# Kernel optimization log

Hardware: AMD Instinct MI355X
Metric: run time of the kernel (lower is better)

Reference implementation:

```python
import jax, jax.numpy as jnp
import numpy as np


def setup_inputs() -> dict:
    key = jax.random.key(0)
    k1, k2 = jax.random.split(key)
    B, N, M = 16, 4096, 4096
    x1 = jax.random.normal(k1, (B, N, 3), dtype=jnp.float32)
    x2 = jax.random.normal(k2, (B, M, 3), dtype=jnp.float32)
    return {"x1": x1, "x2": x2}


def reference(x1, x2) -> jnp.ndarray:
    # x1: [B, N, 3], x2: [B, M, 3]
    # dist_matrix[b, i, j] = ||x1[b,i] - x2[b,j]||^2 via |a|^2 + |b|^2 - 2 a.b
    x1_norm = jnp.sum(x1 * x1, axis=2, keepdims=True)           # [B, N, 1]
    x2_norm = jnp.sum(x2 * x2, axis=2)[:, None, :]              # [B, 1, M]
    cross = jnp.einsum('bnd,bmd->bnm', x1, x2)                  # [B, N, M]
    dist_matrix = x1_norm + x2_norm - 2.0 * cross               # [B, N, M]
    min_1_to_2 = jnp.min(dist_matrix, axis=2)                   # [B, N]
    min_2_to_1 = jnp.min(dist_matrix, axis=1)                   # [B, M]
    chamfer = jnp.mean(min_1_to_2, axis=1) + jnp.mean(min_2_to_1, axis=1)  # [B]
    return chamfer
```

## Files before the change

kernel.cpp:

```cpp
#include <hip/hip_runtime.h>


typedef __attribute__((ext_vector_type(8))) __bf16 bf16x8;
typedef __attribute__((ext_vector_type(16))) float f32x16;

#define PTS 4096
#define NB 16

__device__ __forceinline__ unsigned f2bf(float f) {
  unsigned u = __float_as_uint(f);
  return (u + 0x7FFFu + ((u >> 16) & 1u)) >> 16;
}
__device__ __forceinline__ float bf2f(unsigned s) {
  return __uint_as_float(s << 16);
}
__device__ __forceinline__ unsigned pk(unsigned lo, unsigned hi) {
  return (lo & 0xFFFFu) | (hi << 16);
}

__global__ __launch_bounds__(512, 2) void chamfer_main(
    const float* __restrict__ x1, const float* __restrict__ x2,
    float* __restrict__ rowpart) {
  const int s  = blockIdx.x;
  const int d  = s & 1;
  const int b  = (s >> 1) & (NB - 1);
  const int ch = (s >> 5) & 1;
  const int rg = blockIdx.y;

  const int tid  = threadIdx.x;
  const int lane = tid & 63;
  const int half = lane >> 5;
  const int l31  = lane & 31;
  const int wave = tid >> 6;

  __shared__ uint4 lds[4096];

  const float* Q = d ? x1 : x2;
  const int cbase = b * PTS + ch * 2048;
#pragma unroll
  for (int k = 0; k < 4; ++k) {
    const int j = tid + k * 512;
    const float* q = Q + (size_t)(cbase + j) * 3;
    const float x = q[0], y = q[1], z = q[2];
    const float sx = -2.f * x, sy = -2.f * y, sz = -2.f * z;
    const unsigned Hx = f2bf(sx), Hy = f2bf(sy), Hz = f2bf(sz);
    const unsigned Lx = f2bf(sx - bf2f(Hx));
    const unsigned Ly = f2bf(sy - bf2f(Hy));
    const unsigned Lz = f2bf(sz - bf2f(Hz));
    const float n = fmaf(x, x, fmaf(y, y, z * z));
    const unsigned nh = f2bf(n), nl = f2bf(n - bf2f(nh));
    const unsigned one = 0x3F80u;
    uint4 w0, w1;
    w0.x = pk(Hx, Hy); w0.y = pk(Hz, Lx); w0.z = pk(Ly, Lz); w0.w = pk(Hx, Hy);
    w1.x = pk(Hz, nh); w1.y = pk(nl, one); w1.z = pk(one, 0u); w1.w = 0u;
    lds[(j >> 5) * 64 + (j & 31)]      = w0;
    lds[(j >> 5) * 64 + 32 + (j & 31)] = w1;
  }

  const float* P = d ? x2 : x1;
  const int t0 = rg * 16 + wave * 2;
  bf16x8 af[2];
#pragma unroll
  for (int rr = 0; rr < 2; ++rr) {
    const int r = (t0 + rr) * 32 + l31;
    const float* p = P + (size_t)(b * PTS + r) * 3;
    const float x = p[0], y = p[1], zc = p[2];
    const unsigned hx = f2bf(x), hy = f2bf(y), hz = f2bf(zc);
    const unsigned lx = f2bf(x - bf2f(hx));
    const unsigned ly = f2bf(y - bf2f(hy));
    const unsigned lz = f2bf(zc - bf2f(hz));
    const float n = fmaf(x, x, fmaf(y, y, zc * zc));
    const unsigned nh = f2bf(n), nl = f2bf(n - bf2f(nh));
    const unsigned one = 0x3F80u;
    uint4 w0, w1;
    w0.x = pk(hx, hy); w0.y = pk(hz, hx); w0.z = pk(hy, hz); w0.w = pk(lx, ly);
    w1.x = pk(lz, one); w1.y = pk(one, nh); w1.z = pk(nl, 0u); w1.w = 0u;
    uint4 w;
    w.x = half ? w1.x : w0.x; w.y = half ? w1.y : w0.y;
    w.z = half ? w1.z : w0.z; w.w = half ? w1.w : w0.w;
    af[rr] = *(const bf16x8*)&w;
  }
  const bf16x8 af0 = af[0], af1 = af[1];

  f32x16 zero;
#pragma unroll
  for (int e = 0; e < 16; ++e) zero[e] = 0.f;

  float rm0[16], rm1[16];
#pragma unroll
  for (int e = 0; e < 16; ++e) { rm0[e] = 3.0e38f; rm1[e] = 3.0e38f; }

  __syncthreads();

  const uint4* tp = &lds[half * 32 + l31];
  bf16x8 buf[4];
  buf[0] = *(const bf16x8*)&tp[0];
  buf[1] = *(const bf16x8*)&tp[64];

#pragma unroll 2
  for (int g = 0; g < 32; ++g) {
    const int cur = (g & 1) * 2;
    const int nxt = ((g + 1) & 1) * 2;
    const int pf  = ((g + 1) & 31) * 2;
    buf[nxt]     = *(const bf16x8*)&tp[pf * 64];
    buf[nxt + 1] = *(const bf16x8*)&tp[(pf + 1) * 64];
    const bf16x8 b0 = buf[cur], b1 = buf[cur + 1];
    const f32x16 a00 =
        __builtin_amdgcn_mfma_f32_32x32x16_bf16(af0, b0, zero, 0, 0, 0);
    const f32x16 a01 =
        __builtin_amdgcn_mfma_f32_32x32x16_bf16(af0, b1, zero, 0, 0, 0);
#pragma unroll
    for (int e = 0; e < 16; ++e)
      rm0[e] = fminf(fminf(a00[e], a01[e]), rm0[e]);
    const f32x16 a10 =
        __builtin_amdgcn_mfma_f32_32x32x16_bf16(af1, b0, zero, 0, 0, 0);
    const f32x16 a11 =
        __builtin_amdgcn_mfma_f32_32x32x16_bf16(af1, b1, zero, 0, 0, 0);
#pragma unroll
    for (int e = 0; e < 16; ++e)
      rm1[e] = fminf(fminf(a10[e], a11[e]), rm1[e]);
  }

  float* rbase = rowpart + ((size_t)((ch * 2 + d) * NB + b)) * PTS + t0 * 32;
#pragma unroll
  for (int e = 0; e < 16; ++e) {
    float v = rm0[e];
    v = fminf(v, __shfl_xor(v, 1));
    v = fminf(v, __shfl_xor(v, 2));
    v = fminf(v, __shfl_xor(v, 4));
    v = fminf(v, __shfl_xor(v, 8));
    v = fminf(v, __shfl_xor(v, 16));
    if (l31 == e) {
      const int rl = (e & 3) + 8 * (e >> 2) + 4 * half;
      rbase[rl] = fmaxf(v, 0.f);
    }
  }
#pragma unroll
  for (int e = 0; e < 16; ++e) {
    float v = rm1[e];
    v = fminf(v, __shfl_xor(v, 1));
    v = fminf(v, __shfl_xor(v, 2));
    v = fminf(v, __shfl_xor(v, 4));
    v = fminf(v, __shfl_xor(v, 8));
    v = fminf(v, __shfl_xor(v, 16));
    if (l31 == e) {
      const int rl = 32 + (e & 3) + 8 * (e >> 2) + 4 * half;
      rbase[rl] = fmaxf(v, 0.f);
    }
  }
}

__global__ __launch_bounds__(512) void reduce_rows(
    const float* __restrict__ rowpart, float* __restrict__ out) {
  const int b = blockIdx.x;
  const int tid = threadIdx.x;
  const float* p0 = rowpart + (size_t)(0 * NB + b) * PTS;
  const float* p1 = rowpart + (size_t)(1 * NB + b) * PTS;
  const float* p2 = rowpart + (size_t)(2 * NB + b) * PTS;
  const float* p3 = rowpart + (size_t)(3 * NB + b) * PTS;
  float s = 0.f;
  for (int i = tid; i < PTS; i += 512)
    s += fminf(p0[i], p2[i]) + fminf(p1[i], p3[i]);
  s += __shfl_xor(s, 1);
  s += __shfl_xor(s, 2);
  s += __shfl_xor(s, 4);
  s += __shfl_xor(s, 8);
  s += __shfl_xor(s, 16);
  s += __shfl_xor(s, 32);
  __shared__ float acc[8];
  if ((tid & 63) == 0) acc[tid >> 6] = s;
  __syncthreads();
  if (tid == 0) {
    float t = 0.f;
#pragma unroll
    for (int w = 0; w < 8; ++w) t += acc[w];
    out[b] = t * (1.f / PTS);
  }
}

extern "C" void kernel_launch(void* const* d_in, const int* in_sizes, int n_in,
                              void* d_out, int out_size, void* d_ws,
                              size_t ws_size, hipStream_t stream) {
  const float* x1 = (const float*)d_in[0];
  const float* x2 = (const float*)d_in[1];
  float* out = (float*)d_out;

  float* rowpart = (float*)d_ws;

  dim3 grid(64, 8);
  chamfer_main<<<grid, 512, 0, stream>>>(x1, x2, rowpart);
  reduce_rows<<<NB, 512, 0, stream>>>(rowpart, out);
}
```

Measured before the change: 81.22 us.

## Fuse row reduction into main kernel via global atomic counter tail blocks

Removes the separate reduce_rows launch. Each block bumps a global counter after writing its row minima, and the last 16 arrivals wait for all 512 blocks to finish before reducing one batch each. This saves a kernel launch and its gap, at the cost of atomic stores and loads, a spin-wait, and the assumption that all blocks can make progress. The counter is never reset; it relies on wrapping in multiples of 512.

```diff
diff --git a/kernel.cpp b/kernel.cpp
--- a/kernel.cpp
+++ b/kernel.cpp
@@ -6,6 +6,8 @@
 
 #define PTS 4096
 #define NB 16
+
+__device__ unsigned g_cnt = 0;
 
 __device__ __forceinline__ unsigned f2bf(float f) {
   unsigned u = __float_as_uint(f);
@@ -18,9 +20,9 @@
   return (lo & 0xFFFFu) | (hi << 16);
 }
 
-__global__ __launch_bounds__(512, 2) void chamfer_main(
+__global__ __launch_bounds__(512, 2) void chamfer_all(
     const float* __restrict__ x1, const float* __restrict__ x2,
-    float* __restrict__ rowpart) {
+    float* __restrict__ rowpart, float* __restrict__ out) {
   const int s  = blockIdx.x;
   const int d  = s & 1;
   const int b  = (s >> 1) & (NB - 1);
@@ -121,7 +123,8 @@
       rm1[e] = fminf(fminf(a10[e], a11[e]), rm1[e]);
   }
 
-  float* rbase = rowpart + ((size_t)((ch * 2 + d) * NB + b)) * PTS + t0 * 32;
+  unsigned* rbase =
+      (unsigned*)(rowpart + ((size_t)((ch * 2 + d) * NB + b)) * PTS + t0 * 32);
 #pragma unroll
   for (int e = 0; e < 16; ++e) {
     float v = rm0[e];
@@ -132,7 +135,8 @@
     v = fminf(v, __shfl_xor(v, 16));
     if (l31 == e) {
       const int rl = (e & 3) + 8 * (e >> 2) + 4 * half;
-      rbase[rl] = fmaxf(v, 0.f);
+      __hip_atomic_store(rbase + rl, __float_as_uint(fmaxf(v, 0.f)),
+                         __ATOMIC_RELAXED, __HIP_MEMORY_SCOPE_AGENT);
     }
   }
 #pragma unroll
@@ -145,36 +149,59 @@
     v = fminf(v, __shfl_xor(v, 16));
     if (l31 == e) {
       const int rl = 32 + (e & 3) + 8 * (e >> 2) + 4 * half;
-      rbase[rl] = fmaxf(v, 0.f);
+      __hip_atomic_store(rbase + rl, __float_as_uint(fmaxf(v, 0.f)),
+                         __ATOMIC_RELAXED, __HIP_MEMORY_SCOPE_AGENT);
     }
   }
-}
-
-__global__ __launch_bounds__(512) void reduce_rows(
-    const float* __restrict__ rowpart, float* __restrict__ out) {
-  const int b = blockIdx.x;
-  const int tid = threadIdx.x;
-  const float* p0 = rowpart + (size_t)(0 * NB + b) * PTS;
-  const float* p1 = rowpart + (size_t)(1 * NB + b) * PTS;
-  const float* p2 = rowpart + (size_t)(2 * NB + b) * PTS;
-  const float* p3 = rowpart + (size_t)(3 * NB + b) * PTS;
-  float s = 0.f;
-  for (int i = tid; i < PTS; i += 512)
-    s += fminf(p0[i], p2[i]) + fminf(p1[i], p3[i]);
-  s += __shfl_xor(s, 1);
-  s += __shfl_xor(s, 2);
-  s += __shfl_xor(s, 4);
-  s += __shfl_xor(s, 8);
-  s += __shfl_xor(s, 16);
-  s += __shfl_xor(s, 32);
-  __shared__ float acc[8];
-  if ((tid & 63) == 0) acc[tid >> 6] = s;
+
+  __syncthreads();
+  __shared__ unsigned s_old;
+  if (tid == 0)
+    s_old = __hip_atomic_fetch_add(&g_cnt, 1u, __ATOMIC_ACQ_REL,
+                                   __HIP_MEMORY_SCOPE_AGENT);
+  __syncthreads();
+  const unsigned old = s_old;
+  const unsigned idx = old & 511u;
+  if (idx < 512u - NB) return;
+  const int bb = (int)(idx - (512u - NB));
+  const unsigned target = (old - idx) + 512u;
+  if (tid == 0) {
+    while (__hip_atomic_load(&g_cnt, __ATOMIC_ACQUIRE,
+                             __HIP_MEMORY_SCOPE_AGENT) < target)
+      __builtin_amdgcn_s_sleep(1);
+  }
+  __syncthreads();
+
+  unsigned* q0 = (unsigned*)(rowpart + (size_t)(0 * NB + bb) * PTS);
+  unsigned* q1 = (unsigned*)(rowpart + (size_t)(1 * NB + bb) * PTS);
+  unsigned* q2 = (unsigned*)(rowpart + (size_t)(2 * NB + bb) * PTS);
+  unsigned* q3 = (unsigned*)(rowpart + (size_t)(3 * NB + bb) * PTS);
+  float ssum = 0.f;
+  for (int i = tid; i < PTS; i += 512) {
+    const float a0 = __uint_as_float(__hip_atomic_load(
+        q0 + i, __ATOMIC_RELAXED, __HIP_MEMORY_SCOPE_AGENT));
+    const float a1 = __uint_as_float(__hip_atomic_load(
+        q1 + i, __ATOMIC_RELAXED, __HIP_MEMORY_SCOPE_AGENT));
+    const float a2 = __uint_as_float(__hip_atomic_load(
+        q2 + i, __ATOMIC_RELAXED, __HIP_MEMORY_SCOPE_AGENT));
+    const float a3 = __uint_as_float(__hip_atomic_load(
+        q3 + i, __ATOMIC_RELAXED, __HIP_MEMORY_SCOPE_AGENT));
+    ssum += fminf(a0, a2) + fminf(a1, a3);
+  }
+  ssum += __shfl_xor(ssum, 1);
+  ssum += __shfl_xor(ssum, 2);
+  ssum += __shfl_xor(ssum, 4);
+  ssum += __shfl_xor(ssum, 8);
+  ssum += __shfl_xor(ssum, 16);
+  ssum += __shfl_xor(ssum, 32);
+  __shared__ float facc[8];
+  if ((tid & 63) == 0) facc[wave] = ssum;
   __syncthreads();
   if (tid == 0) {
     float t = 0.f;
 #pragma unroll
-    for (int w = 0; w < 8; ++w) t += acc[w];
-    out[b] = t * (1.f / PTS);
+    for (int w = 0; w < 8; ++w) t += facc[w];
+    out[bb] = t * (1.f / PTS);
   }
 }
 
@@ -188,6 +215,5 @@
   float* rowpart = (float*)d_ws;
 
   dim3 grid(64, 8);
-  chamfer_main<<<grid, 512, 0, stream>>>(x1, x2, rowpart);
-  reduce_rows<<<NB, 512, 0, stream>>>(rowpart, out);
-}
+  chamfer_all<<<grid, 512, 0, stream>>>(x1, x2, rowpart, out);
+}
```

New measurement: 84.79 us. 1.04x slower.
